# Optimization experiments

Hardware: AMD Instinct MI355X
Metric: run time of the kernel (lower is better)

The kernel has to match this reference:

```python
import jax, jax.numpy as jnp
import numpy as np

N = 100000      # nodes
E = 1600000     # edges (avg degree 16)
G = 1024        # graphs in the batch
D_IN = 128      # input_size
D_EMB = 128     # embedding_size


def _l2_normalize(x, eps=1e-12):
    # F.normalize(p=2, dim=-1): x / max(||x||_2, eps)
    n = jnp.sqrt(jnp.sum(x * x, axis=-1, keepdims=True))
    return x / jnp.maximum(n, eps)


def setup_inputs() -> dict:
    key = jax.random.key(0)
    ks = jax.random.split(key, 11)
    x = jax.random.normal(ks[0], (N, D_IN), dtype=jnp.float32)
    edge_src = jax.random.randint(ks[1], (E,), 0, N, dtype=jnp.int32)
    edge_dst = jax.random.randint(ks[2], (E,), 0, N, dtype=jnp.int32)
    edge_val = jax.random.uniform(ks[3], (E,), dtype=jnp.float32)  # normalized adjacency weights
    batch_ids = jax.random.randint(ks[4], (N,), 0, G, dtype=jnp.int32)
    batch_val = jax.random.uniform(ks[5], (N,), dtype=jnp.float32)  # pooling weights
    # parameters (xavier-ish scales)
    lim_in = float(np.sqrt(6.0 / (D_IN + D_EMB)))
    lim_e = float(np.sqrt(6.0 / (D_EMB + D_EMB)))
    W_in = jax.random.uniform(ks[6], (D_IN, D_EMB), minval=-lim_in, maxval=lim_in, dtype=jnp.float32)
    b_in = jnp.zeros((D_EMB,), dtype=jnp.float32)
    W_gcn = jax.random.uniform(ks[7], (D_EMB, D_EMB), minval=-lim_e, maxval=lim_e, dtype=jnp.float32)
    W_g = jax.random.uniform(ks[8], (D_EMB, D_EMB), minval=-lim_e, maxval=lim_e, dtype=jnp.float32)
    b_g = jnp.zeros((D_EMB,), dtype=jnp.float32)
    return dict(x=x, edge_src=edge_src, edge_dst=edge_dst, edge_val=edge_val,
                batch_ids=batch_ids, batch_val=batch_val,
                W_in=W_in, b_in=b_in, W_gcn=W_gcn, W_g=W_g, b_g=b_g,
                num_nodes=N, num_graphs=G)


def reference(x, edge_src, edge_dst, edge_val, batch_ids, batch_val,
              W_in, b_in, W_gcn, W_g, b_g, num_nodes, num_graphs):
    # h = relu(fc_input(x))                          [N, D_EMB]
    h = jax.nn.relu(x @ W_in + b_in)
    # h_struct = sparse.mm(A, h) @ W_gcn ; A in COO: out[i] = sum_e val[e]*h[dst[e]] for src[e]==i
    msgs = h[edge_dst] * edge_val[:, None]           # [E, D_EMB]
    agg = jax.ops.segment_sum(msgs, edge_src, num_segments=num_nodes)
    h_struct = _l2_normalize(jax.nn.relu(agg @ W_gcn))
    # h_graph = sparse.mm(B, h_struct): weighted pool of nodes into graphs
    h_graph = jax.ops.segment_sum(h_struct * batch_val[:, None], batch_ids, num_segments=num_graphs)
    h_graph = _l2_normalize(jax.nn.relu(h_graph @ W_g + b_g))
    return (h_struct, h_graph)
```

## Files before the change

### kernel.cpp

```cpp
#include <hip/hip_runtime.h>
#include <hip/hip_bf16.h>

#define D 128
#define CAP 64
#define GCAP 192
#define NBKT 8
#define EPB 512

typedef __attribute__((ext_vector_type(8))) short short8;
typedef __attribute__((ext_vector_type(4))) float f32x4;

__device__ __forceinline__ float b2f(unsigned short u) {
    union { unsigned int i; float f; } v;
    v.i = ((unsigned int)u) << 16;
    return v.f;
}
__device__ __forceinline__ unsigned short f2b(float f) {
    __hip_bfloat16 h = __float2bfloat16(f);
    return __builtin_bit_cast(unsigned short, h);
}

__global__ void k_prep(const float* __restrict__ Wa, unsigned short* __restrict__ Ahi,
                       unsigned short* __restrict__ Alo,
                       const float* __restrict__ Wb, unsigned short* __restrict__ Bhi,
                       unsigned short* __restrict__ Blo) {
    int b = blockIdx.x;
    const float* W = (b < 64) ? Wa : Wb;
    unsigned short* Hi = (b < 64) ? Ahi : Bhi;
    unsigned short* Lo = (b < 64) ? Alo : Blo;
    int i = (b & 63) * 256 + threadIdx.x;
    int k = i >> 7, n = i & 127;
    float w = W[i];
    unsigned short hi = f2b(w);
    unsigned short lo = f2b(w - b2f(hi));
    Hi[n * D + k] = hi;
    Lo[n * D + k] = lo;
}

__global__ __launch_bounds__(256) void k_part(
        const int* __restrict__ esrc, const int* __restrict__ edst,
        const float* __restrict__ eval,
        int* __restrict__ bcur,
        int2* __restrict__ bdv, int* __restrict__ bsrc,
        int bucketCap, int NR, int E,
        const int* __restrict__ bids, const float* __restrict__ bval,
        int* __restrict__ gcnt, int2* __restrict__ gdata, int N) {
    __shared__ int lcnt[NBKT];
    __shared__ int lofs[NBKT];
    __shared__ int lbase[NBKT];
    __shared__ int ltot;
    __shared__ int ssrc[EPB], sdst[EPB], sval[EPB];
    __shared__ unsigned char sbkt[EPB];
    const int tid = threadIdx.x;
    const int i0 = blockIdx.x * EPB + tid;
    const int i1 = i0 + 256;

    if (tid < NBKT) lcnt[tid] = 0;
    __syncthreads();

    int s0 = 0, d0 = 0, v0 = 0, b0 = 0, m0 = -1;
    int s1 = 0, d1 = 0, v1 = 0, b1 = 0, m1 = -1;
    if (i0 < E) {
        s0 = esrc[i0]; d0 = edst[i0]; v0 = __float_as_int(eval[i0]);
        b0 = s0 / NR;
        m0 = atomicAdd(&lcnt[b0], 1);
    }
    if (i1 < E) {
        s1 = esrc[i1]; d1 = edst[i1]; v1 = __float_as_int(eval[i1]);
        b1 = s1 / NR;
        m1 = atomicAdd(&lcnt[b1], 1);
    }
    __syncthreads();

    if (tid == 0) {
        int run = 0;
#pragma unroll
        for (int b = 0; b < NBKT; b++) { lofs[b] = run; run += lcnt[b]; }
        ltot = run;
    }
    if (tid < NBKT) lbase[tid] = atomicAdd(&bcur[tid], lcnt[tid]);
    __syncthreads();

    if (m0 >= 0) {
        int p = lofs[b0] + m0;
        ssrc[p] = s0; sdst[p] = d0; sval[p] = v0; sbkt[p] = (unsigned char)b0;
    }
    if (m1 >= 0) {
        int p = lofs[b1] + m1;
        ssrc[p] = s1; sdst[p] = d1; sval[p] = v1; sbkt[p] = (unsigned char)b1;
    }
    __syncthreads();

    int total = ltot;
    for (int t = tid; t < total; t += 256) {
        int b = sbkt[t];
        int slot = lbase[b] + (t - lofs[b]);
        if (slot < bucketCap) {
            size_t idx = (size_t)b * bucketCap + slot;
            int2 dv; dv.x = sdst[t]; dv.y = sval[t];
            bdv[idx]  = dv;
            bsrc[idx] = ssrc[t];
        }
    }

    if (i0 < N) {
        int g = bids[i0];
        int slot = atomicAdd(&gcnt[g], 1);
        if (slot < GCAP) {
            int2 d; d.x = i0; d.y = __float_as_int(bval[i0]);
            gdata[(size_t)g * GCAP + slot] = d;
        }
    }
    if (i1 < N) {
        int g = bids[i1];
        int slot = atomicAdd(&gcnt[g], 1);
        if (slot < GCAP) {
            int2 d; d.x = i1; d.y = __float_as_int(bval[i1]);
            gdata[(size_t)g * GCAP + slot] = d;
        }
    }
}

__global__ __launch_bounds__(256) void k_scatter3(
        const int* __restrict__ bcur,
        const int2* __restrict__ bdv, const int* __restrict__ bsrc,
        int* __restrict__ cnt, int2* __restrict__ edata, int bucketCap) {
    const int grp = blockIdx.x & 7;
    const int bi = blockIdx.x >> 3;
    const int stride = (gridDim.x >> 3) * 256;
    int nrec = bcur[grp];
    if (nrec > bucketCap) nrec = bucketCap;
    const size_t base = (size_t)grp * bucketCap;

    for (int j = bi * 256 + threadIdx.x; j < nrec; j += stride) {
        int s = bsrc[base + j];
        int2 dv = bdv[base + j];
        int slot = atomicAdd(&cnt[s], 1);
        if (slot < CAP) edata[(size_t)s * CAP + slot] = dv;
    }
}

__global__ __launch_bounds__(256, 3) void k_gemm_fused(
        const float* __restrict__ X,
        const unsigned short* __restrict__ W1hi, const unsigned short* __restrict__ W1lo,
        const float* __restrict__ bias1,
        const unsigned short* __restrict__ W2hi, const unsigned short* __restrict__ W2lo,
        unsigned short* __restrict__ HW, int N) {
    __shared__ __align__(16) char wbuf[2][16384];
    __shared__ float htile_s[4 * 16 * 68];
    const int tid  = threadIdx.x;
    const int wave = tid >> 6;
    const int lane = tid & 63;
    const int q = lane >> 4;
    const int l15 = lane & 15;
    const int lane16 = lane * 16;
    const int row0 = blockIdx.x * 64 + wave * 16;
    float* tile = htile_s + wave * 16 * 68;

    int arow = row0 + l15;
    if (arow >= N) arow = N - 1;
    const float* xrow = X + (size_t)arow * D;

    uint4 r0, r1, r2, r3;
#define LOAD_WCHUNK(Whi, Wlo, kkc)                                              \
    {                                                                           \
        int s0 = tid, s1 = tid + 256;                                           \
        int t0_ = s0 >> 6, q0_ = (s0 >> 4) & 3, l0_ = s0 & 15;                  \
        int t1_ = s1 >> 6, q1_ = (s1 >> 4) & 3, l1_ = s1 & 15;                  \
        size_t g0 = (size_t)(t0_ * 16 + l0_) * 256 + (kkc) * 64 + q0_ * 16;     \
        size_t g1 = (size_t)(t1_ * 16 + l1_) * 256 + (kkc) * 64 + q1_ * 16;     \
        r0 = *(const uint4*)((const char*)(Whi) + g0);                          \
        r1 = *(const uint4*)((const char*)(Whi) + g1);                          \
        r2 = *(const uint4*)((const char*)(Wlo) + g0);                          \
        r3 = *(const uint4*)((const char*)(Wlo) + g1);                          \
    }
#define STORE_WCHUNK(buf)                                                       \
    {                                                                           \
        ((uint4*)(buf))[tid] = r0;                                              \
        ((uint4*)(buf))[tid + 256] = r1;                                        \
        ((uint4*)((buf) + 8192))[tid] = r2;                                     \
        ((uint4*)((buf) + 8192))[tid + 256] = r3;                               \
    }

    LOAD_WCHUNK(W1hi, W1lo, 0);

    short8 xhi[4], xlo[4];
#pragma unroll
    for (int kk = 0; kk < 4; kk++) {
        float4 f0 = *(const float4*)(xrow + kk * 32 + q * 8);
        float4 f1 = *(const float4*)(xrow + kk * 32 + q * 8 + 4);
        float fv[8] = {f0.x, f0.y, f0.z, f0.w, f1.x, f1.y, f1.z, f1.w};
#pragma unroll
        for (int j = 0; j < 8; j++) {
            unsigned short h = f2b(fv[j]);
            xhi[kk][j] = (short)h;
            xlo[kk][j] = (short)f2b(fv[j] - b2f(h));
        }
    }

    STORE_WCHUNK(wbuf[0]);

    f32x4 acc[8];
#pragma unroll
    for (int t = 0; t < 8; t++) acc[t] = (f32x4){0.f, 0.f, 0.f, 0.f};

#pragma unroll
    for (int kk = 0; kk < 4; kk++) {
        __syncthreads();
        if (kk < 3) { LOAD_WCHUNK(W1hi, W1lo, kk + 1); }
        else        { LOAD_WCHUNK(W2hi, W2lo, 0); }
        const char* cb = wbuf[kk & 1];
#pragma unroll
        for (int t = 0; t < 8; t++) {
            short8 bhi = *(const short8*)(cb + t * 1024 + lane16);
            short8 blo = *(const short8*)(cb + 8192 + t * 1024 + lane16);
            acc[t] = __builtin_amdgcn_mfma_f32_16x16x32_bf16(xhi[kk], bhi, acc[t], 0, 0, 0);
            acc[t] = __builtin_amdgcn_mfma_f32_16x16x32_bf16(xhi[kk], blo, acc[t], 0, 0, 0);
            acc[t] = __builtin_amdgcn_mfma_f32_16x16x32_bf16(xlo[kk], bhi, acc[t], 0, 0, 0);
        }
        STORE_WCHUNK(wbuf[(kk + 1) & 1]);
    }

    f32x4 acc2[8];
#pragma unroll
    for (int t = 0; t < 8; t++) acc2[t] = (f32x4){0.f, 0.f, 0.f, 0.f};

#pragma unroll
    for (int hf = 0; hf < 2; hf++) {
#pragma unroll
        for (int tt = 0; tt < 4; tt++) {
            int t = hf * 4 + tt;
            int col = t * 16 + l15;
            float bv = bias1[col];
#pragma unroll
            for (int rr = 0; rr < 4; rr++) {
                float v = acc[t][rr] + bv;
                v = v > 0.f ? v : 0.f;
                tile[(q * 4 + rr) * 68 + tt * 16 + l15] = v;
            }
        }
#pragma unroll
        for (int kk2 = 0; kk2 < 2; kk2++) {
            int c = hf * 2 + kk2;
            __syncthreads();
            if (c < 3) { LOAD_WCHUNK(W2hi, W2lo, c + 1); }
            const float* hp = tile + l15 * 68 + kk2 * 32 + q * 8;
            float4 f0 = *(const float4*)(hp);
            float4 f1 = *(const float4*)(hp + 4);
            float fv[8] = {f0.x, f0.y, f0.z, f0.w, f1.x, f1.y, f1.z, f1.w};
            short8 ahi, alo;
#pragma unroll
            for (int j = 0; j < 8; j++) {
                unsigned short h = f2b(fv[j]);
                ahi[j] = (short)h;
                alo[j] = (short)f2b(fv[j] - b2f(h));
            }
            const char* cb = wbuf[c & 1];
#pragma unroll
            for (int t2 = 0; t2 < 8; t2++) {
                short8 bhi = *(const short8*)(cb + t2 * 1024 + lane16);
                short8 blo = *(const short8*)(cb + 8192 + t2 * 1024 + lane16);
                acc2[t2] = __builtin_amdgcn_mfma_f32_16x16x32_bf16(ahi, bhi, acc2[t2], 0, 0, 0);
                acc2[t2] = __builtin_amdgcn_mfma_f32_16x16x32_bf16(ahi, blo, acc2[t2], 0, 0, 0);
                acc2[t2] = __builtin_amdgcn_mfma_f32_16x16x32_bf16(alo, bhi, acc2[t2], 0, 0, 0);
            }
            if (c < 3) { STORE_WCHUNK(wbuf[(c + 1) & 1]); }
        }
    }

#pragma unroll
    for (int t = 0; t < 8; t++) {
        int col = t * 16 + l15;
#pragma unroll
        for (int rr = 0; rr < 4; rr++) {
            int row = row0 + q * 4 + rr;
            if (row < N) {
                unsigned short hv = f2b(acc2[t][rr]);
                __builtin_nontemporal_store(hv, &HW[(size_t)row * D + col]);
            }
        }
    }
#undef LOAD_WCHUNK
#undef STORE_WCHUNK
}

__global__ __launch_bounds__(256) void k_agg_finalize(
        const int* __restrict__ cnt, const int2* __restrict__ edata,
        const unsigned int* __restrict__ hw32,
        float* __restrict__ hstruct, int N) {
    const int lane = threadIdx.x & 63;
    const int wave = threadIdx.x >> 6;
    const int nA = blockIdx.x * 8 + wave * 2;
    const int nB = nA + 1;
    if (nA >= N) return;
    int degA = cnt[nA]; if (degA > CAP) degA = CAP;
    int degB = 0;
    if (nB < N) { degB = cnt[nB]; if (degB > CAP) degB = CAP; }
    const int2* epA = edata + (size_t)nA * CAP;
    const int2* epB = edata + (size_t)nB * CAP;

    float a0 = 0.f, a1 = 0.f, c0v = 0.f, c1v = 0.f;
    int ja = 0, jb = 0;

    while (ja + 4 <= degA && jb + 4 <= degB) {
        int2 ea0 = epA[ja], ea1 = epA[ja + 1], ea2 = epA[ja + 2], ea3 = epA[ja + 3];
        int2 eb0 = epB[jb], eb1 = epB[jb + 1], eb2 = epB[jb + 2], eb3 = epB[jb + 3];
        unsigned int pa0 = hw32[(size_t)ea0.x * 64 + lane];
        unsigned int pa1 = hw32[(size_t)ea1.x * 64 + lane];
        unsigned int pa2 = hw32[(size_t)ea2.x * 64 + lane];
        unsigned int pa3 = hw32[(size_t)ea3.x * 64 + lane];
        unsigned int pb0 = hw32[(size_t)eb0.x * 64 + lane];
        unsigned int pb1 = hw32[(size_t)eb1.x * 64 + lane];
        unsigned int pb2 = hw32[(size_t)eb2.x * 64 + lane];
        unsigned int pb3 = hw32[(size_t)eb3.x * 64 + lane];
        a0 = fmaf(__int_as_float(ea0.y), b2f((unsigned short)(pa0 & 0xffffu)), a0);
        a1 = fmaf(__int_as_float(ea0.y), b2f((unsigned short)(pa0 >> 16)), a1);
        a0 = fmaf(__int_as_float(ea1.y), b2f((unsigned short)(pa1 & 0xffffu)), a0);
        a1 = fmaf(__int_as_float(ea1.y), b2f((unsigned short)(pa1 >> 16)), a1);
        a0 = fmaf(__int_as_float(ea2.y), b2f((unsigned short)(pa2 & 0xffffu)), a0);
        a1 = fmaf(__int_as_float(ea2.y), b2f((unsigned short)(pa2 >> 16)), a1);
        a0 = fmaf(__int_as_float(ea3.y), b2f((unsigned short)(pa3 & 0xffffu)), a0);
        a1 = fmaf(__int_as_float(ea3.y), b2f((unsigned short)(pa3 >> 16)), a1);
        c0v = fmaf(__int_as_float(eb0.y), b2f((unsigned short)(pb0 & 0xffffu)), c0v);
        c1v = fmaf(__int_as_float(eb0.y), b2f((unsigned short)(pb0 >> 16)), c1v);
        c0v = fmaf(__int_as_float(eb1.y), b2f((unsigned short)(pb1 & 0xffffu)), c0v);
        c1v = fmaf(__int_as_float(eb1.y), b2f((unsigned short)(pb1 >> 16)), c1v);
        c0v = fmaf(__int_as_float(eb2.y), b2f((unsigned short)(pb2 & 0xffffu)), c0v);
        c1v = fmaf(__int_as_float(eb2.y), b2f((unsigned short)(pb2 >> 16)), c1v);
        c0v = fmaf(__int_as_float(eb3.y), b2f((unsigned short)(pb3 & 0xffffu)), c0v);
        c1v = fmaf(__int_as_float(eb3.y), b2f((unsigned short)(pb3 >> 16)), c1v);
        ja += 4; jb += 4;
    }
    for (; ja + 4 <= degA; ja += 4) {
        int2 e0 = epA[ja], e1 = epA[ja + 1], e2 = epA[ja + 2], e3 = epA[ja + 3];
        unsigned int p0 = hw32[(size_t)e0.x * 64 + lane];
        unsigned int p1 = hw32[(size_t)e1.x * 64 + lane];
        unsigned int p2 = hw32[(size_t)e2.x * 64 + lane];
        unsigned int p3 = hw32[(size_t)e3.x * 64 + lane];
        a0 = fmaf(__int_as_float(e0.y), b2f((unsigned short)(p0 & 0xffffu)), a0);
        a1 = fmaf(__int_as_float(e0.y), b2f((unsigned short)(p0 >> 16)), a1);
        a0 = fmaf(__int_as_float(e1.y), b2f((unsigned short)(p1 & 0xffffu)), a0);
        a1 = fmaf(__int_as_float(e1.y), b2f((unsigned short)(p1 >> 16)), a1);
        a0 = fmaf(__int_as_float(e2.y), b2f((unsigned short)(p2 & 0xffffu)), a0);
        a1 = fmaf(__int_as_float(e2.y), b2f((unsigned short)(p2 >> 16)), a1);
        a0 = fmaf(__int_as_float(e3.y), b2f((unsigned short)(p3 & 0xffffu)), a0);
        a1 = fmaf(__int_as_float(e3.y), b2f((unsigned short)(p3 >> 16)), a1);
    }
    for (; ja < degA; ja++) {
        int2 e = epA[ja];
        unsigned int p = hw32[(size_t)e.x * 64 + lane];
        a0 = fmaf(__int_as_float(e.y), b2f((unsigned short)(p & 0xffffu)), a0);
        a1 = fmaf(__int_as_float(e.y), b2f((unsigned short)(p >> 16)), a1);
    }
    for (; jb + 4 <= degB; jb += 4) {
        int2 e0 = epB[jb], e1 = epB[jb + 1], e2 = epB[jb + 2], e3 = epB[jb + 3];
        unsigned int p0 = hw32[(size_t)e0.x * 64 + lane];
        unsigned int p1 = hw32[(size_t)e1.x * 64 + lane];
        unsigned int p2 = hw32[(size_t)e2.x * 64 + lane];
        unsigned int p3 = hw32[(size_t)e3.x * 64 + lane];
        c0v = fmaf(__int_as_float(e0.y), b2f((unsigned short)(p0 & 0xffffu)), c0v);
        c1v = fmaf(__int_as_float(e0.y), b2f((unsigned short)(p0 >> 16)), c1v);
        c0v = fmaf(__int_as_float(e1.y), b2f((unsigned short)(p1 & 0xffffu)), c0v);
        c1v = fmaf(__int_as_float(e1.y), b2f((unsigned short)(p1 >> 16)), c1v);
        c0v = fmaf(__int_as_float(e2.y), b2f((unsigned short)(p2 & 0xffffu)), c0v);
        c1v = fmaf(__int_as_float(e2.y), b2f((unsigned short)(p2 >> 16)), c1v);
        c0v = fmaf(__int_as_float(e3.y), b2f((unsigned short)(p3 & 0xffffu)), c0v);
        c1v = fmaf(__int_as_float(e3.y), b2f((unsigned short)(p3 >> 16)), c1v);
    }
    for (; jb < degB; jb++) {
        int2 e = epB[jb];
        unsigned int p = hw32[(size_t)e.x * 64 + lane];
        c0v = fmaf(__int_as_float(e.y), b2f((unsigned short)(p & 0xffffu)), c0v);
        c1v = fmaf(__int_as_float(e.y), b2f((unsigned short)(p >> 16)), c1v);
    }

    a0 = a0 > 0.f ? a0 : 0.f;
    a1 = a1 > 0.f ? a1 : 0.f;
    float ssA = a0 * a0 + a1 * a1;
#pragma unroll
    for (int m = 1; m < 64; m <<= 1) ssA += __shfl_xor(ssA, m, 64);
    float scA = 1.0f / fmaxf(sqrtf(ssA), 1e-12f);
    float2 oA; oA.x = a0 * scA; oA.y = a1 * scA;
    __builtin_nontemporal_store(__builtin_bit_cast(double, oA),
                                (double*)(hstruct + (size_t)nA * D + 2 * lane));

    if (nB < N) {
        c0v = c0v > 0.f ? c0v : 0.f;
        c1v = c1v > 0.f ? c1v : 0.f;
        float ssB = c0v * c0v + c1v * c1v;
#pragma unroll
        for (int m = 1; m < 64; m <<= 1) ssB += __shfl_xor(ssB, m, 64);
        float scB = 1.0f / fmaxf(sqrtf(ssB), 1e-12f);
        float2 oB; oB.x = c0v * scB; oB.y = c1v * scB;
        __builtin_nontemporal_store(__builtin_bit_cast(double, oB),
                                    (double*)(hstruct + (size_t)nB * D + 2 * lane));
    }
}

__global__ __launch_bounds__(256) void k_graph_finalize(
        const int* __restrict__ gcnt, const int2* __restrict__ gdata,
        const float* __restrict__ hstruct,
        const float* __restrict__ Wg, const float* __restrict__ bg,
        float* __restrict__ out, int G) {
    __shared__ float part[4][128];
    __shared__ float part2[4][128];
    const int lane = threadIdx.x & 63;
    const int wave = threadIdx.x >> 6;
    const int g = blockIdx.x;
    if (g >= G) return;
    const int c0 = 2 * lane;

    int deg = gcnt[g];
    if (deg > GCAP) deg = GCAP;
    const int2* gd = gdata + (size_t)g * GCAP;

    float a0 = 0.f, a1 = 0.f;
    int idx = wave;
    for (; idx + 28 < deg; idx += 32) {
        int2 e0 = gd[idx],      e1 = gd[idx + 4],  e2 = gd[idx + 8],  e3 = gd[idx + 12];
        int2 e4 = gd[idx + 16], e5 = gd[idx + 20], e6 = gd[idx + 24], e7 = gd[idx + 28];
        float2 h0 = *(const float2*)(hstruct + (size_t)e0.x * D + c0);
        float2 h1 = *(const float2*)(hstruct + (size_t)e1.x * D + c0);
        float2 h2 = *(const float2*)(hstruct + (size_t)e2.x * D + c0);
        float2 h3 = *(const float2*)(hstruct + (size_t)e3.x * D + c0);
        float2 h4 = *(const float2*)(hstruct + (size_t)e4.x * D + c0);
        float2 h5 = *(const float2*)(hstruct + (size_t)e5.x * D + c0);
        float2 h6 = *(const float2*)(hstruct + (size_t)e6.x * D + c0);
        float2 h7 = *(const float2*)(hstruct + (size_t)e7.x * D + c0);
        a0 = fmaf(__int_as_float(e0.y), h0.x, a0);
        a1 = fmaf(__int_as_float(e0.y), h0.y, a1);
        a0 = fmaf(__int_as_float(e1.y), h1.x, a0);
        a1 = fmaf(__int_as_float(e1.y), h1.y, a1);
        a0 = fmaf(__int_as_float(e2.y), h2.x, a0);
        a1 = fmaf(__int_as_float(e2.y), h2.y, a1);
        a0 = fmaf(__int_as_float(e3.y), h3.x, a0);
        a1 = fmaf(__int_as_float(e3.y), h3.y, a1);
        a0 = fmaf(__int_as_float(e4.y), h4.x, a0);
        a1 = fmaf(__int_as_float(e4.y), h4.y, a1);
        a0 = fmaf(__int_as_float(e5.y), h5.x, a0);
        a1 = fmaf(__int_as_float(e5.y), h5.y, a1);
        a0 = fmaf(__int_as_float(e6.y), h6.x, a0);
        a1 = fmaf(__int_as_float(e6.y), h6.y, a1);
        a0 = fmaf(__int_as_float(e7.y), h7.x, a0);
        a1 = fmaf(__int_as_float(e7.y), h7.y, a1);
    }
    for (; idx < deg; idx += 4) {
        int2 e = gd[idx];
        float2 hs = *(const float2*)(hstruct + (size_t)e.x * D + c0);
        a0 = fmaf(__int_as_float(e.y), hs.x, a0);
        a1 = fmaf(__int_as_float(e.y), hs.y, a1);
    }
    part[wave][c0]     = a0;
    part[wave][c0 + 1] = a1;
    __syncthreads();
    a0 = part[0][c0]     + part[1][c0]     + part[2][c0]     + part[3][c0];
    a1 = part[0][c0 + 1] + part[1][c0 + 1] + part[2][c0 + 1] + part[3][c0 + 1];

    float o0 = 0.f, o1 = 0.f;
#pragma unroll 2
    for (int kq = 0; kq < 32; kq++) {
        int k = wave * 32 + kq;
        float xv = (k & 1) ? __shfl(a1, k >> 1, 64) : __shfl(a0, k >> 1, 64);
        float2 w = *(const float2*)(Wg + (size_t)k * D + c0);
        o0 = fmaf(xv, w.x, o0);
        o1 = fmaf(xv, w.y, o1);
    }
    part2[wave][c0]     = o0;
    part2[wave][c0 + 1] = o1;
    __syncthreads();
    if (wave == 0) {
        o0 = part2[0][c0]     + part2[1][c0]     + part2[2][c0]     + part2[3][c0];
        o1 = part2[0][c0 + 1] + part2[1][c0 + 1] + part2[2][c0 + 1] + part2[3][c0 + 1];
        o0 += bg[c0];
        o1 += bg[c0 + 1];
        o0 = o0 > 0.f ? o0 : 0.f;
        o1 = o1 > 0.f ? o1 : 0.f;
        float ss = o0 * o0 + o1 * o1;
#pragma unroll
        for (int m = 1; m < 64; m <<= 1) ss += __shfl_xor(ss, m, 64);
        float scale = 1.0f / fmaxf(sqrtf(ss), 1e-12f);
        float2 o; o.x = o0 * scale; o.y = o1 * scale;
        *(float2*)(out + (size_t)g * D + c0) = o;
    }
}

extern "C" void kernel_launch(void* const* d_in, const int* in_sizes, int n_in,
                              void* d_out, int out_size, void* d_ws, size_t ws_size,
                              hipStream_t stream) {
    const float* x     = (const float*)d_in[0];
    const int*   esrc  = (const int*)d_in[1];
    const int*   edst  = (const int*)d_in[2];
    const float* eval  = (const float*)d_in[3];
    const int*   bids  = (const int*)d_in[4];
    const float* bval  = (const float*)d_in[5];
    const float* W_in  = (const float*)d_in[6];
    const float* b_in  = (const float*)d_in[7];
    const float* W_gcn = (const float*)d_in[8];
    const float* W_g   = (const float*)d_in[9];
    const float* b_g   = (const float*)d_in[10];

    const int N = in_sizes[4];
    const int E = in_sizes[1];
    const int G = 1024;

    const int NR = (N + NBKT - 1) / NBKT;
    const int bucketCap = E / NBKT + E / 64;

    auto pad = [](size_t v) { return (v + 255) & ~(size_t)255; };
    char* ws = (char*)d_ws;
    unsigned short* whi_in  = (unsigned short*)ws; ws += pad((size_t)D * D * 2);
    unsigned short* wlo_in  = (unsigned short*)ws; ws += pad((size_t)D * D * 2);
    unsigned short* whi_gcn = (unsigned short*)ws; ws += pad((size_t)D * D * 2);
    unsigned short* wlo_gcn = (unsigned short*)ws; ws += pad((size_t)D * D * 2);
    int*   cnt    = (int*)ws;  ws += pad((size_t)N * 4);
    int*   gcnt   = (int*)ws;  ws += pad((size_t)G * 4);
    int*   bcur   = (int*)ws;  ws += pad((size_t)NBKT * 4);
    unsigned short* hw = (unsigned short*)ws; ws += pad((size_t)N * D * 2);
    int2*  edata  = (int2*)ws; ws += pad((size_t)N * CAP * 8);
    int2*  gdata  = (int2*)ws; ws += pad((size_t)G * GCAP * 8);
    int2*  bdv    = (int2*)ws; ws += pad((size_t)NBKT * bucketCap * 8);
    int*   bsrc   = (int*)ws;  ws += pad((size_t)NBKT * bucketCap * 4);

    hipMemsetAsync(cnt, 0, (size_t)((char*)bcur - (char*)cnt) + pad((size_t)NBKT * 4), stream);

    k_prep<<<128, 256, 0, stream>>>(W_in, whi_in, wlo_in, W_gcn, whi_gcn, wlo_gcn);

    int mb = ((E > N ? E : N) + EPB - 1) / EPB;
    k_part<<<mb, 256, 0, stream>>>(esrc, edst, eval, bcur, bdv, bsrc,
                                   bucketCap, NR, E, bids, bval, gcnt, gdata, N);
    k_scatter3<<<2048, 256, 0, stream>>>(bcur, bdv, bsrc, cnt, edata, bucketCap);

    const int gb = (N + 63) / 64;
    k_gemm_fused<<<gb, 256, 0, stream>>>(x, whi_in, wlo_in, b_in,
                                         whi_gcn, wlo_gcn, hw, N);

    float* hstruct = (float*)d_out;
    float* hgraph  = hstruct + (size_t)N * D;

    k_agg_finalize<<<(N + 7) / 8, 256, 0, stream>>>(cnt, edata,
                                                    (const unsigned int*)hw, hstruct, N);
    k_graph_finalize<<<G, 256, 0, stream>>>(gcnt, gdata, hstruct, W_g, b_g, hgraph, G);
}
```

Baseline: 376.1 us.

## Split each wave into half-waves processing alternate edges with 8-byte gathers

The aggregation kernel now splits each 64-lane wave into two 32-lane halves. Each half handles every other edge of a node and loads 4 bf16 features (8 bytes) per lane instead of 2, and edge records are read as 16-byte pairs. The two halves' partial sums are combined with a cross-half shuffle before ReLU and normalization. Output is written with one 16-byte store per lane from the lower half. This gives wider, fewer gather transactions and more edges in flight per wave, at the cost of extra shuffles, per-lane selects and idle upper-half lanes during the store.

```diff
diff --git a/kernel.cpp b/kernel.cpp
--- a/kernel.cpp
+++ b/kernel.cpp
@@ -290,6 +290,8 @@
         float* __restrict__ hstruct, int N) {
     const int lane = threadIdx.x & 63;
     const int wave = threadIdx.x >> 6;
+    const int half = lane >> 5;
+    const int l5 = lane & 31;
     const int nA = blockIdx.x * 8 + wave * 2;
     const int nB = nA + 1;
     if (nA >= N) return;
@@ -298,102 +300,132 @@
     if (nB < N) { degB = cnt[nB]; if (degB > CAP) degB = CAP; }
     const int2* epA = edata + (size_t)nA * CAP;
     const int2* epB = edata + (size_t)nB * CAP;
-
-    float a0 = 0.f, a1 = 0.f, c0v = 0.f, c1v = 0.f;
+    const unsigned int* hwl = hw32 + l5 * 2;
+
+    float a0 = 0.f, a1 = 0.f, a2 = 0.f, a3 = 0.f;
+    float b0 = 0.f, b1 = 0.f, b2 = 0.f, b3 = 0.f;
     int ja = 0, jb = 0;
 
+#define PAIR_FMA(p, vv, x0, x1, x2, x3)                                         \
+    x0 = fmaf(vv, b2f((unsigned short)((p).x & 0xffffu)), x0);                  \
+    x1 = fmaf(vv, b2f((unsigned short)((p).x >> 16)), x1);                      \
+    x2 = fmaf(vv, b2f((unsigned short)((p).y & 0xffffu)), x2);                  \
+    x3 = fmaf(vv, b2f((unsigned short)((p).y >> 16)), x3);
+
     while (ja + 4 <= degA && jb + 4 <= degB) {
-        int2 ea0 = epA[ja], ea1 = epA[ja + 1], ea2 = epA[ja + 2], ea3 = epA[ja + 3];
-        int2 eb0 = epB[jb], eb1 = epB[jb + 1], eb2 = epB[jb + 2], eb3 = epB[jb + 3];
-        unsigned int pa0 = hw32[(size_t)ea0.x * 64 + lane];
-        unsigned int pa1 = hw32[(size_t)ea1.x * 64 + lane];
-        unsigned int pa2 = hw32[(size_t)ea2.x * 64 + lane];
-        unsigned int pa3 = hw32[(size_t)ea3.x * 64 + lane];
-        unsigned int pb0 = hw32[(size_t)eb0.x * 64 + lane];
-        unsigned int pb1 = hw32[(size_t)eb1.x * 64 + lane];
-        unsigned int pb2 = hw32[(size_t)eb2.x * 64 + lane];
-        unsigned int pb3 = hw32[(size_t)eb3.x * 64 + lane];
-        a0 = fmaf(__int_as_float(ea0.y), b2f((unsigned short)(pa0 & 0xffffu)), a0);
-        a1 = fmaf(__int_as_float(ea0.y), b2f((unsigned short)(pa0 >> 16)), a1);
-        a0 = fmaf(__int_as_float(ea1.y), b2f((unsigned short)(pa1 & 0xffffu)), a0);
-        a1 = fmaf(__int_as_float(ea1.y), b2f((unsigned short)(pa1 >> 16)), a1);
-        a0 = fmaf(__int_as_float(ea2.y), b2f((unsigned short)(pa2 & 0xffffu)), a0);
-        a1 = fmaf(__int_as_float(ea2.y), b2f((unsigned short)(pa2 >> 16)), a1);
-        a0 = fmaf(__int_as_float(ea3.y), b2f((unsigned short)(pa3 & 0xffffu)), a0);
-        a1 = fmaf(__int_as_float(ea3.y), b2f((unsigned short)(pa3 >> 16)), a1);
-        c0v = fmaf(__int_as_float(eb0.y), b2f((unsigned short)(pb0 & 0xffffu)), c0v);
-        c1v = fmaf(__int_as_float(eb0.y), b2f((unsigned short)(pb0 >> 16)), c1v);
-        c0v = fmaf(__int_as_float(eb1.y), b2f((unsigned short)(pb1 & 0xffffu)), c0v);
-        c1v = fmaf(__int_as_float(eb1.y), b2f((unsigned short)(pb1 >> 16)), c1v);
-        c0v = fmaf(__int_as_float(eb2.y), b2f((unsigned short)(pb2 & 0xffffu)), c0v);
-        c1v = fmaf(__int_as_float(eb2.y), b2f((unsigned short)(pb2 >> 16)), c1v);
-        c0v = fmaf(__int_as_float(eb3.y), b2f((unsigned short)(pb3 & 0xffffu)), c0v);
-        c1v = fmaf(__int_as_float(eb3.y), b2f((unsigned short)(pb3 >> 16)), c1v);
+        int4 rA0 = *(const int4*)(epA + ja);
+        int4 rA1 = *(const int4*)(epA + ja + 2);
+        int4 rB0 = *(const int4*)(epB + jb);
+        int4 rB1 = *(const int4*)(epB + jb + 2);
+        int djA0 = half ? rA0.z : rA0.x;
+        int djA1 = half ? rA1.z : rA1.x;
+        int djB0 = half ? rB0.z : rB0.x;
+        int djB1 = half ? rB1.z : rB1.x;
+        uint2 pA0 = *(const uint2*)(hwl + (size_t)djA0 * 64);
+        uint2 pA1 = *(const uint2*)(hwl + (size_t)djA1 * 64);
+        uint2 pB0 = *(const uint2*)(hwl + (size_t)djB0 * 64);
+        uint2 pB1 = *(const uint2*)(hwl + (size_t)djB1 * 64);
+        float vA0 = __int_as_float(half ? rA0.w : rA0.y);
+        float vA1 = __int_as_float(half ? rA1.w : rA1.y);
+        float vB0 = __int_as_float(half ? rB0.w : rB0.y);
+        float vB1 = __int_as_float(half ? rB1.w : rB1.y);
+        PAIR_FMA(pA0, vA0, a0, a1, a2, a3)
+        PAIR_FMA(pA1, vA1, a0, a1, a2, a3)
+        PAIR_FMA(pB0, vB0, b0, b1, b2, b3)
+        PAIR_FMA(pB1, vB1, b0, b1, b2, b3)
         ja += 4; jb += 4;
     }
     for (; ja + 4 <= degA; ja += 4) {
-        int2 e0 = epA[ja], e1 = epA[ja + 1], e2 = epA[ja + 2], e3 = epA[ja + 3];
-        unsigned int p0 = hw32[(size_t)e0.x * 64 + lane];
-        unsigned int p1 = hw32[(size_t)e1.x * 64 + lane];
-        unsigned int p2 = hw32[(size_t)e2.x * 64 + lane];
-        unsigned int p3 = hw32[(size_t)e3.x * 64 + lane];
-        a0 = fmaf(__int_as_float(e0.y), b2f((unsigned short)(p0 & 0xffffu)), a0);
-        a1 = fmaf(__int_as_float(e0.y), b2f((unsigned short)(p0 >> 16)), a1);
-        a0 = fmaf(__int_as_float(e1.y), b2f((unsigned short)(p1 & 0xffffu)), a0);
-        a1 = fmaf(__int_as_float(e1.y), b2f((unsigned short)(p1 >> 16)), a1);
-        a0 = fmaf(__int_as_float(e2.y), b2f((unsigned short)(p2 & 0xffffu)), a0);
-        a1 = fmaf(__int_as_float(e2.y), b2f((unsigned short)(p2 >> 16)), a1);
-        a0 = fmaf(__int_as_float(e3.y), b2f((unsigned short)(p3 & 0xffffu)), a0);
-        a1 = fmaf(__int_as_float(e3.y), b2f((unsigned short)(p3 >> 16)), a1);
-    }
-    for (; ja < degA; ja++) {
-        int2 e = epA[ja];
-        unsigned int p = hw32[(size_t)e.x * 64 + lane];
-        a0 = fmaf(__int_as_float(e.y), b2f((unsigned short)(p & 0xffffu)), a0);
-        a1 = fmaf(__int_as_float(e.y), b2f((unsigned short)(p >> 16)), a1);
+        int4 r0 = *(const int4*)(epA + ja);
+        int4 r1 = *(const int4*)(epA + ja + 2);
+        int dj0 = half ? r0.z : r0.x;
+        int dj1 = half ? r1.z : r1.x;
+        uint2 p0 = *(const uint2*)(hwl + (size_t)dj0 * 64);
+        uint2 p1 = *(const uint2*)(hwl + (size_t)dj1 * 64);
+        float v0 = __int_as_float(half ? r0.w : r0.y);
+        float v1 = __int_as_float(half ? r1.w : r1.y);
+        PAIR_FMA(p0, v0, a0, a1, a2, a3)
+        PAIR_FMA(p1, v1, a0, a1, a2, a3)
+    }
+    for (; ja + 2 <= degA; ja += 2) {
+        int2 e0 = epA[ja], e1 = epA[ja + 1];
+        int dj = half ? e1.x : e0.x;
+        float vv = __int_as_float(half ? e1.y : e0.y);
+        uint2 p = *(const uint2*)(hwl + (size_t)dj * 64);
+        PAIR_FMA(p, vv, a0, a1, a2, a3)
+    }
+    if (ja < degA) {
+        int2 e0 = epA[ja];
+        int dj = e0.x;
+        float vv = half ? 0.f : __int_as_float(e0.y);
+        uint2 p = *(const uint2*)(hwl + (size_t)dj * 64);
+        PAIR_FMA(p, vv, a0, a1, a2, a3)
     }
     for (; jb + 4 <= degB; jb += 4) {
-        int2 e0 = epB[jb], e1 = epB[jb + 1], e2 = epB[jb + 2], e3 = epB[jb + 3];
-        unsigned int p0 = hw32[(size_t)e0.x * 64 + lane];
-        unsigned int p1 = hw32[(size_t)e1.x * 64 + lane];
-        unsigned int p2 = hw32[(size_t)e2.x * 64 + lane];
-        unsigned int p3 = hw32[(size_t)e3.x * 64 + lane];
-        c0v = fmaf(__int_as_float(e0.y), b2f((unsigned short)(p0 & 0xffffu)), c0v);
-        c1v = fmaf(__int_as_float(e0.y), b2f((unsigned short)(p0 >> 16)), c1v);
-        c0v = fmaf(__int_as_float(e1.y), b2f((unsigned short)(p1 & 0xffffu)), c0v);
-        c1v = fmaf(__int_as_float(e1.y), b2f((unsigned short)(p1 >> 16)), c1v);
-        c0v = fmaf(__int_as_float(e2.y), b2f((unsigned short)(p2 & 0xffffu)), c0v);
-        c1v = fmaf(__int_as_float(e2.y), b2f((unsigned short)(p2 >> 16)), c1v);
-        c0v = fmaf(__int_as_float(e3.y), b2f((unsigned short)(p3 & 0xffffu)), c0v);
-        c1v = fmaf(__int_as_float(e3.y), b2f((unsigned short)(p3 >> 16)), c1v);
-    }
-    for (; jb < degB; jb++) {
-        int2 e = epB[jb];
-        unsigned int p = hw32[(size_t)e.x * 64 + lane];
-        c0v = fmaf(__int_as_float(e.y), b2f((unsigned short)(p & 0xffffu)), c0v);
-        c1v = fmaf(__int_as_float(e.y), b2f((unsigned short)(p >> 16)), c1v);
-    }
+        int4 r0 = *(const int4*)(epB + jb);
+        int4 r1 = *(const int4*)(epB + jb + 2);
+        int dj0 = half ? r0.z : r0.x;
+        int dj1 = half ? r1.z : r1.x;
+        uint2 p0 = *(const uint2*)(hwl + (size_t)dj0 * 64);
+        uint2 p1 = *(const uint2*)(hwl + (size_t)dj1 * 64);
+        float v0 = __int_as_float(half ? r0.w : r0.y);
+        float v1 = __int_as_float(half ? r1.w : r1.y);
+        PAIR_FMA(p0, v0, b0, b1, b2, b3)
+        PAIR_FMA(p1, v1, b0, b1, b2, b3)
+    }
+    for (; jb + 2 <= degB; jb += 2) {
+        int2 e0 = epB[jb], e1 = epB[jb + 1];
+        int dj = half ? e1.x : e0.x;
+        float vv = __int_as_float(half ? e1.y : e0.y);
+        uint2 p = *(const uint2*)(hwl + (size_t)dj * 64);
+        PAIR_FMA(p, vv, b0, b1, b2, b3)
+    }
+    if (jb < degB) {
+        int2 e0 = epB[jb];
+        int dj = e0.x;
+        float vv = half ? 0.f : __int_as_float(e0.y);
+        uint2 p = *(const uint2*)(hwl + (size_t)dj * 64);
+        PAIR_FMA(p, vv, b0, b1, b2, b3)
+    }
+#undef PAIR_FMA
+
+    a0 += __shfl_xor(a0, 32, 64);
+    a1 += __shfl_xor(a1, 32, 64);
+    a2 += __shfl_xor(a2, 32, 64);
+    a3 += __shfl_xor(a3, 32, 64);
 
     a0 = a0 > 0.f ? a0 : 0.f;
     a1 = a1 > 0.f ? a1 : 0.f;
-    float ssA = a0 * a0 + a1 * a1;
-#pragma unroll
-    for (int m = 1; m < 64; m <<= 1) ssA += __shfl_xor(ssA, m, 64);
+    a2 = a2 > 0.f ? a2 : 0.f;
+    a3 = a3 > 0.f ? a3 : 0.f;
+    float ssA = a0 * a0 + a1 * a1 + a2 * a2 + a3 * a3;
+#pragma unroll
+    for (int m = 1; m < 32; m <<= 1) ssA += __shfl_xor(ssA, m, 64);
     float scA = 1.0f / fmaxf(sqrtf(ssA), 1e-12f);
-    float2 oA; oA.x = a0 * scA; oA.y = a1 * scA;
-    __builtin_nontemporal_store(__builtin_bit_cast(double, oA),
-                                (double*)(hstruct + (size_t)nA * D + 2 * lane));
+    if (half == 0) {
+        f32x4 oA;
+        oA[0] = a0 * scA; oA[1] = a1 * scA; oA[2] = a2 * scA; oA[3] = a3 * scA;
+        __builtin_nontemporal_store(oA, (f32x4*)(hstruct + (size_t)nA * D + 4 * l5));
+    }
 
     if (nB < N) {
-        c0v = c0v > 0.f ? c0v : 0.f;
-        c1v = c1v > 0.f ? c1v : 0.f;
-        float ssB = c0v * c0v + c1v * c1v;
-#pragma unroll
-        for (int m = 1; m < 64; m <<= 1) ssB += __shfl_xor(ssB, m, 64);
+        b0 += __shfl_xor(b0, 32, 64);
+        b1 += __shfl_xor(b1, 32, 64);
+        b2 += __shfl_xor(b2, 32, 64);
+        b3 += __shfl_xor(b3, 32, 64);
+        b0 = b0 > 0.f ? b0 : 0.f;
+        b1 = b1 > 0.f ? b1 : 0.f;
+        b2 = b2 > 0.f ? b2 : 0.f;
+        b3 = b3 > 0.f ? b3 : 0.f;
+        float ssB = b0 * b0 + b1 * b1 + b2 * b2 + b3 * b3;
+#pragma unroll
+        for (int m = 1; m < 32; m <<= 1) ssB += __shfl_xor(ssB, m, 64);
         float scB = 1.0f / fmaxf(sqrtf(ssB), 1e-12f);
-        float2 oB; oB.x = c0v * scB; oB.y = c1v * scB;
-        __builtin_nontemporal_store(__builtin_bit_cast(double, oB),
-                                    (double*)(hstruct + (size_t)nB * D + 2 * lane));
+        if (half == 0) {
+            f32x4 oB;
+            oB[0] = b0 * scB; oB[1] = b1 * scB; oB[2] = b2 * scB; oB[3] = b3 * scB;
+            __builtin_nontemporal_store(oB, (f32x4*)(hstruct + (size_t)nB * D + 4 * l5));
+        }
     }
 }
 
```

Measured after the change: 378.5 us. No clear change (+0.6%).
